# Kernel optimization log

Measured on AMD Instinct MI355X. Metric: run time of the kernel, lower is better.

The kernel has to match this reference:

```python
import jax, jax.numpy as jnp
import numpy as np
from jax import lax

M = 8192  # number of candidate detections
C = 80    # number of classes (COCO)
MIN_CONF = 0.25
MIN_IOU = 0.45
VALID_CLASS_IDS = jnp.array([2, 3, 5, 7], dtype=jnp.int32)  # COCO vehicles


def setup_inputs() -> dict:
    key = jax.random.key(0)
    k1, k2, k3, k4, k5, k6, k7 = jax.random.split(key, 7)
    # boxes stored as (y1, x1, y2, x2) in input-image pixel space, guaranteed y1<y2, x1<x2
    y1 = jax.random.uniform(k1, (1, M)) * 600.0
    x1 = jax.random.uniform(k2, (1, M)) * 600.0
    h = jax.random.uniform(k3, (1, M)) * 120.0 + 4.0
    w = jax.random.uniform(k4, (1, M)) * 120.0 + 4.0
    boxes_raw = jnp.stack([y1, x1, y1 + h, x1 + w], axis=-1).astype(jnp.float32)  # [1,M,4]
    scores = jax.random.uniform(k5, (1, C, M), dtype=jnp.float32)  # [1,C,M]
    cls = jax.random.randint(k6, (1, M), 0, C, dtype=jnp.int32)
    idx = jax.random.randint(k7, (1, M), 0, M, dtype=jnp.int32)
    indices = jnp.stack([jnp.zeros_like(cls), cls, idx], axis=-1)  # [1,M,3]: (batch, class_id, box_idx)
    return {"boxes_raw": boxes_raw, "scores": scores, "indices": indices, "out_h": 640, "out_w": 640}


def _pairwise_iou(b):
    # b: [M,4] (x1,y1,x2,y2)
    x1, y1, x2, y2 = b[:, 0], b[:, 1], b[:, 2], b[:, 3]
    area = jnp.maximum(x2 - x1, 0.0) * jnp.maximum(y2 - y1, 0.0)  # [M]
    ix1 = jnp.maximum(x1[:, None], x1[None, :])
    iy1 = jnp.maximum(y1[:, None], y1[None, :])
    ix2 = jnp.minimum(x2[:, None], x2[None, :])
    iy2 = jnp.minimum(y2[:, None], y2[None, :])
    inter = jnp.maximum(ix2 - ix1, 0.0) * jnp.maximum(iy2 - iy1, 0.0)  # [M,M]
    return inter / (area[:, None] + area[None, :] - inter + 1e-9)


def _postprocess(boxes_raw, scores, indices, out_h, out_w):
    idxs = indices[0, :, 2]       # predicted-positive box indices [M]
    class_ids = indices[0, :, 1]  # class ids [M]
    conf = scores[0, class_ids, idxs]  # irregular gather [M]
    b = boxes_raw[0, idxs]  # [M,4] (y1,x1,y2,x2)
    # swap to (x1,y1,x2,y2) as in the original column permutation
    boxes = jnp.stack([b[:, 1], b[:, 0], b[:, 3], b[:, 2]], axis=-1)
    bounds = jnp.array([out_w, out_h, out_w, out_h], dtype=boxes.dtype)
    boxes = jnp.clip(boxes, 0.0, bounds)  # clip_boxes to output image size
    # confidence filter + class filter (as masks; static shapes)
    valid = (conf > MIN_CONF) & jnp.isin(class_ids, VALID_CLASS_IDS)
    # class-agnostic greedy NMS over valid detections
    s = jnp.where(valid, conf, -1.0)
    order = jnp.argsort(-s)  # descending score
    sb = boxes[order]
    sv = valid[order]
    iou = _pairwise_iou(sb)  # [M,M]
    rng = jnp.arange(M)

    def body(i, keep):
        suppress = keep[i] & (iou[i] > MIN_IOU) & (rng > i)
        return keep & ~suppress

    keep_sorted = lax.fori_loop(0, M, body, sv)
    keep = jnp.zeros((M,), dtype=bool).at[order].set(keep_sorted)
    boxes_out = boxes * keep[:, None].astype(boxes.dtype)
    conf_out = conf * keep.astype(conf.dtype)
    return boxes_out, conf_out, class_ids.astype(jnp.int64), keep


def reference(boxes_raw, scores, indices, out_h, out_w):
    return _postprocess(boxes_raw, scores, indices, out_h, out_w)
```

## Files before the change

kernel.cpp:

```cpp
#include <hip/hip_runtime.h>
#include <stdint.h>

#define M_BOXES 8192
#define MIN_CONF_F 0.25f
#define MIN_IOU_F 0.45f
#define VCAP 640
#define NW 10
#define NBLKB 32
#define FLAG_MAGIC 0x5EEDF00D

typedef unsigned long long u64;
typedef unsigned int u32;

#define WS_FLAGS  0
#define WS_WCNT   512
#define WS_VKEYS  1024
#define WS_SUP    66560
#define WS_NEED   117760

__device__ inline float scalar_to_float(const int* p) {
    int v = p[0];
    if (v > 0 && v < (1 << 20)) return (float)v;
    return __int_as_float(v);
}

__device__ inline u64 rl64(u64 v, int b) {
    u32 lo = (u32)__builtin_amdgcn_readlane((int)(u32)v, b);
    u32 hi = (u32)__builtin_amdgcn_readlane((int)(u32)(v >> 32), b);
    return ((u64)hi << 32) | lo;
}

__device__ inline u64 rfl64(u64 v) {
    u32 lo = (u32)__builtin_amdgcn_readfirstlane((int)(u32)v);
    u32 hi = (u32)__builtin_amdgcn_readfirstlane((int)(u32)(v >> 32));
    return ((u64)hi << 32) | lo;
}

__device__ inline u64 wave_or64(u64 v) {
    #pragma unroll
    for (int o = 32; o > 0; o >>= 1) {
        int lo = __shfl_xor((int)(u32)v, o, 64);
        int hi = __shfl_xor((int)(u32)(v >> 32), o, 64);
        v |= ((u64)(u32)hi << 32) | (u32)lo;
    }
    return v;
}

__global__ __launch_bounds__(512) void kA_gather(
    const float* __restrict__ scores, const int* __restrict__ indices,
    float* __restrict__ out, u64* __restrict__ vkeys, int* __restrict__ wcnt)
{
    int tid = threadIdx.x;
    int i = blockIdx.x * 512 + tid;
    int cls = indices[3 * i + 1];
    int idx = indices[3 * i + 2];
    float conf = scores[cls * M_BOXES + idx];
    *reinterpret_cast<float4*>(out + 4 * i) = make_float4(0.f, 0.f, 0.f, 0.f);
    out[4 * M_BOXES + i] = 0.f;
    out[5 * M_BOXES + i] = (float)cls;
    out[6 * M_BOXES + i] = 0.f;
    bool valid = (conf > MIN_CONF_F) &&
                 (cls == 2 || cls == 3 || cls == 5 || cls == 7);
    u64 mask = __ballot(valid);
    int lane = tid & 63;
    int wid = i >> 6;
    if (valid) {
        int pos = (int)__popcll(mask & ((1ull << lane) - 1ull));
        u64 key = ((u64)(~__float_as_uint(conf)) << 32)
                | ((u64)(u32)i << 13) | (u64)(u32)idx;
        vkeys[(wid << 6) + pos] = key;
    }
    if (lane == 0) wcnt[wid] = (int)__popcll(mask);
}

__global__ __launch_bounds__(512) void kB_all(
    const float* __restrict__ boxes_raw, const int* __restrict__ p_out_h,
    const int* __restrict__ p_out_w, float* __restrict__ out,
    const u64* __restrict__ vkeys, const int* __restrict__ wcnt,
    u64* __restrict__ sup, int* __restrict__ flags)
{
    __shared__ int pre_s[129];
    __shared__ u64 tkey[VCAP];
    __shared__ u64 skey_s[VCAP];
    __shared__ float4 sbox_s[VCAP];
    __shared__ float sarea_s[VCAP];
    __shared__ u64 live_s[NW];

    int tid = threadIdx.x, b = blockIdx.x;
    int widx = tid >> 6, lane = tid & 63;

    if (tid < 64) {
        int cA = wcnt[tid], cB = wcnt[64 + tid];
        int sA = cA, sB = cB;
        #pragma unroll
        for (int o = 1; o < 64; o <<= 1) {
            int t = __shfl_up(sA, o, 64); if (tid >= o) sA += t;
            int u = __shfl_up(sB, o, 64); if (tid >= o) sB += u;
        }
        int totA = __shfl(sA, 63, 64);
        int totB = __shfl(sB, 63, 64);
        pre_s[tid] = sA - cA;
        pre_s[64 + tid] = totA + sB - cB;
        if (tid == 0) pre_s[128] = totA + totB;
    }
    __syncthreads();
    int V = pre_s[128];
    if (V > VCAP) V = VCAP;

    if (V > 0) {
        for (int s = tid; s < V; s += 512) {
            int lo = 0, hi = 128;
            #pragma unroll
            for (int st = 0; st < 7; ++st) {
                int mid = (lo + hi) >> 1;
                if (pre_s[mid] <= s) lo = mid; else hi = mid;
            }
            tkey[s] = vkeys[(lo << 6) + (s - pre_s[lo])];
        }
        __syncthreads();

        float W = scalar_to_float(p_out_w);
        float H = scalar_to_float(p_out_h);
        for (int s = tid; s < V; s += 512) {
            u64 k = tkey[s];
            int bidx = (int)(k & 0x1FFFull);
            float4 bb = *reinterpret_cast<const float4*>(boxes_raw + 4 * bidx);
            int r = 0;
            #pragma unroll 4
            for (int j = 0; j < V; ++j) r += (tkey[j] < k) ? 1 : 0;
            float4 c4;
            c4.x = fminf(fmaxf(bb.y, 0.f), W);
            c4.y = fminf(fmaxf(bb.x, 0.f), H);
            c4.z = fminf(fmaxf(bb.w, 0.f), W);
            c4.w = fminf(fmaxf(bb.z, 0.f), H);
            skey_s[r] = k;
            sbox_s[r] = c4;
            sarea_s[r] = fmaxf(c4.z - c4.x, 0.f) * fmaxf(c4.w - c4.y, 0.f);
        }
        __syncthreads();

        int nw = (V + 63) >> 6;
        int nbi = (V + 7) >> 3;
        int ntask = nbi * nw;
        int gw = (b << 3) + widx;
        for (int t = gw; t < ntask; t += NBLKB * 8) {
            int bi = t / nw;
            int w = t - bi * nw;
            int i0 = bi << 3;
            int j = (w << 6) + lane;
            bool jv = j < V;
            float4 bj = jv ? sbox_s[j] : make_float4(0.f, 0.f, 0.f, 0.f);
            float aj = jv ? sarea_s[j] : 0.f;
            int rend = V - i0; if (rend > 8) rend = 8;
            for (int r = 0; r < rend; ++r) {
                int i = i0 + r;
                float4 bi4 = sbox_s[i];
                float ai = sarea_s[i];
                bool p = false;
                if (jv && j > i) {
                    float ix1 = fmaxf(bi4.x, bj.x);
                    float iy1 = fmaxf(bi4.y, bj.y);
                    float ix2 = fminf(bi4.z, bj.z);
                    float iy2 = fminf(bi4.w, bj.w);
                    float inter = fmaxf(ix2 - ix1, 0.f) * fmaxf(iy2 - iy1, 0.f);
                    float iou = inter / (ai + aj - inter + 1e-9f);
                    p = iou > MIN_IOU_F;
                }
                u64 bits = __ballot(p);
                if (lane == 0) sup[i * NW + w] = bits;
            }
        }
    }

    __syncthreads();
    if (tid == 0) {
        __threadfence();
        __hip_atomic_store(&flags[b], FLAG_MAGIC, __ATOMIC_RELEASE,
                           __HIP_MEMORY_SCOPE_AGENT);
    }
    if (b != 0) return;
    if (tid < NBLKB) {
        while (__hip_atomic_load(&flags[tid], __ATOMIC_ACQUIRE,
                                 __HIP_MEMORY_SCOPE_AGENT) != FLAG_MAGIC)
            __builtin_amdgcn_s_sleep(1);
    }
    __syncthreads();
    __threadfence();

    if (V > 0) {
        int nw = (V + 63) >> 6;
        if (tid < 64) {
            u64 live[NW], supp[NW];
            #pragma unroll
            for (int w = 0; w < NW; ++w) {
                int c = V - (w << 6);
                live[w] = (c >= 64) ? ~0ull : (c > 0 ? ((1ull << c) - 1ull) : 0ull);
                supp[w] = 0ull;
            }
            u64 rowA[NW], rowB[NW];
            {
                bool rv = lane < V;
                #pragma unroll
                for (int w = 0; w < NW; ++w)
                    rowA[w] = (rv && w < nw) ? sup[lane * NW + w] : 0ull;
            }
            auto step = [&](u64 (&rc)[NW], u64 (&rn)[NW], int ci) {
                int rI = ((ci + 1) << 6) + lane;
                bool rv = (ci + 1) < nw && rI < V;
                #pragma unroll
                for (int w = 0; w < NW; ++w)
                    rn[w] = (rv && w >= ci + 1 && w < nw) ? sup[rI * NW + w] : 0ull;
                u64 rw = 0, cur = 0;
                #pragma unroll
                for (int w = 0; w < NW; ++w)
                    if (w == ci) { rw = rc[w]; cur = live[w] & ~supp[w]; }
                cur = rfl64(cur);
                #pragma unroll
                for (int bb = 0; bb < 64; ++bb) {
                    u64 rb = rl64(rw, bb);
                    u64 nxt = cur & ~rb;
                    cur = ((cur >> bb) & 1ull) ? nxt : cur;
                }
                #pragma unroll
                for (int w = 0; w < NW; ++w) if (w == ci) live[w] = cur;
                #pragma unroll
                for (int w2 = 0; w2 < NW; ++w2)
                    if (w2 > ci && w2 < nw) {
                        u64 mine = ((cur >> lane) & 1ull) ? rc[w2] : 0ull;
                        supp[w2] |= rfl64(wave_or64(mine));
                    }
            };
            int ci = 0;
            while (ci < nw) {
                step(rowA, rowB, ci); ++ci;
                if (ci < nw) { step(rowB, rowA, ci); ++ci; }
            }
            #pragma unroll
            for (int w = 0; w < NW; ++w) live_s[w] = live[w];
        }
        __syncthreads();
        for (int s = tid; s < V; s += 512) {
            if ((live_s[s >> 6] >> (s & 63)) & 1ull) {
                u64 k = skey_s[s];
                u32 orig = (u32)((k >> 13) & 0x1FFFull);
                float conf = __uint_as_float(~(u32)(k >> 32));
                float4 bb = sbox_s[s];
                *reinterpret_cast<float4*>(out + 4 * orig) = bb;
                out[4 * M_BOXES + orig] = conf;
                out[6 * M_BOXES + orig] = 1.0f;
            }
        }
    }

    if (tid < NBLKB)
        __hip_atomic_store(&flags[tid], 0, __ATOMIC_RELEASE,
                           __HIP_MEMORY_SCOPE_AGENT);
}

__global__ __launch_bounds__(256) void fb_gather(
    const float* __restrict__ boxes_raw, const float* __restrict__ scores,
    const int* __restrict__ indices, const int* __restrict__ p_out_h,
    const int* __restrict__ p_out_w, float* __restrict__ out,
    u64* __restrict__ vkeys, float4* __restrict__ vboxes,
    int* __restrict__ vcount)
{
    int i = blockIdx.x * blockDim.x + threadIdx.x;
    if (i >= M_BOXES) return;
    int cls = indices[3 * i + 1];
    int idx = indices[3 * i + 2];
    float conf = scores[cls * M_BOXES + idx];
    *reinterpret_cast<float4*>(out + 4 * i) = make_float4(0.f, 0.f, 0.f, 0.f);
    out[4 * M_BOXES + i] = 0.f;
    out[5 * M_BOXES + i] = (float)cls;
    out[6 * M_BOXES + i] = 0.f;
    bool valid = (conf > MIN_CONF_F) &&
                 (cls == 2 || cls == 3 || cls == 5 || cls == 7);
    if (valid) {
        float4 bb = *reinterpret_cast<const float4*>(boxes_raw + 4 * idx);
        float W = scalar_to_float(p_out_w);
        float H = scalar_to_float(p_out_h);
        float4 c;
        c.x = fminf(fmaxf(bb.y, 0.f), W);
        c.y = fminf(fmaxf(bb.x, 0.f), H);
        c.z = fminf(fmaxf(bb.w, 0.f), W);
        c.w = fminf(fmaxf(bb.z, 0.f), H);
        int p = atomicAdd(vcount, 1);
        if (p < VCAP) {
            vkeys[p] = ((u64)(~__float_as_uint(conf)) << 32) | (u32)i;
            vboxes[p] = c;
        }
    }
}

__global__ __launch_bounds__(1024) void fb_nms(
    float* __restrict__ out, const u64* __restrict__ vkeys,
    const float4* __restrict__ vboxes, const int* __restrict__ vcount)
{
    __shared__ u64 tkey[VCAP];
    __shared__ u64 skey[VCAP];
    __shared__ float4 sbox[VCAP];
    __shared__ unsigned char keepb[VCAP];
    int tid = threadIdx.x;
    int V = *vcount;
    if (V > VCAP) V = VCAP;
    if (V <= 0) return;
    for (int s = tid; s < V; s += 1024) tkey[s] = vkeys[s];
    __syncthreads();
    for (int s = tid; s < V; s += 1024) {
        u64 k = tkey[s];
        int r = 0;
        for (int j = 0; j < V; ++j) r += (tkey[j] < k);
        skey[r] = k;
        sbox[r] = vboxes[s];
    }
    __syncthreads();
    for (int s = tid; s < V; s += 1024) keepb[s] = 1;
    __syncthreads();
    for (int i = 0; i < V; ++i) {
        if (keepb[i]) {
            float4 bi = sbox[i];
            float ai = fmaxf(bi.z - bi.x, 0.f) * fmaxf(bi.w - bi.y, 0.f);
            for (int s = i + 1 + tid; s < V; s += 1024) {
                if (keepb[s]) {
                    float4 bj = sbox[s];
                    float aj = fmaxf(bj.z - bj.x, 0.f) * fmaxf(bj.w - bj.y, 0.f);
                    float ix1 = fmaxf(bi.x, bj.x);
                    float iy1 = fmaxf(bi.y, bj.y);
                    float ix2 = fminf(bi.z, bj.z);
                    float iy2 = fminf(bi.w, bj.w);
                    float inter = fmaxf(ix2 - ix1, 0.f) * fmaxf(iy2 - iy1, 0.f);
                    float iou = inter / (ai + aj - inter + 1e-9f);
                    if (iou > MIN_IOU_F) keepb[s] = 0;
                }
            }
        }
        __syncthreads();
    }
    for (int s = tid; s < V; s += 1024) {
        if (keepb[s]) {
            u64 k = skey[s];
            u32 orig = (u32)(k & 0xFFFFFFFFull);
            float conf = __uint_as_float(~(u32)(k >> 32));
            float4 bb = sbox[s];
            *reinterpret_cast<float4*>(out + 4 * orig) = bb;
            out[4 * M_BOXES + orig] = conf;
            out[6 * M_BOXES + orig] = 1.0f;
        }
    }
}

extern "C" void kernel_launch(void* const* d_in, const int* in_sizes, int n_in,
                              void* d_out, int out_size, void* d_ws, size_t ws_size,
                              hipStream_t stream) {
    const float* boxes_raw = (const float*)d_in[0];
    const float* scores    = (const float*)d_in[1];
    const int*   indices   = (const int*)d_in[2];
    const int*   p_out_h   = (const int*)d_in[3];
    const int*   p_out_w   = (const int*)d_in[4];
    float* out = (float*)d_out;
    char* ws = (char*)d_ws;

    if (ws_size >= WS_NEED) {
        int* flags = (int*)(ws + WS_FLAGS);
        int* wcnt  = (int*)(ws + WS_WCNT);
        u64* vkeys = (u64*)(ws + WS_VKEYS);
        u64* sup   = (u64*)(ws + WS_SUP);

        kA_gather<<<M_BOXES / 512, 512, 0, stream>>>(
            scores, indices, out, vkeys, wcnt);
        kB_all<<<NBLKB, 512, 0, stream>>>(
            boxes_raw, p_out_h, p_out_w, out, vkeys, wcnt, sup, flags);
    } else {
        int*    vcount = (int*)ws;
        u64*    vkeys  = (u64*)(ws + 16);
        float4* vboxes = (float4*)(ws + 16 + VCAP * sizeof(u64));
        hipMemsetAsync(d_ws, 0, 16, stream);
        fb_gather<<<M_BOXES / 256, 256, 0, stream>>>(
            boxes_raw, scores, indices, p_out_h, p_out_w, out,
            vkeys, vboxes, vcount);
        fb_nms<<<1, 1024, 0, stream>>>(out, vkeys, vboxes, vcount);
    }
}
```

Baseline: 35.41 us.

## Fuse gather kernel into NMS kernel with a grid-wide flag barrier

Merges the score gather/compaction kernel into the main NMS kernel. Each of the 32 blocks gathers 256 candidates, then all blocks spin on a second set of release/acquire flags before the prefix scan. This removes one kernel launch and the inter-kernel gap, at the cost of a software grid barrier that only works if all 32 blocks are co-resident. Half of each block's threads sit idle during the gather phase.

New measurement: 38.18 us. 1.08x slower.

```diff
diff --git a/kernel.cpp b/kernel.cpp
--- a/kernel.cpp
+++ b/kernel.cpp
@@ -6,13 +6,14 @@
 #define MIN_IOU_F 0.45f
 #define VCAP 640
 #define NW 10
-#define NBLKB 32
+#define NBLK 32
 #define FLAG_MAGIC 0x5EEDF00D
 
 typedef unsigned long long u64;
 typedef unsigned int u32;
 
-#define WS_FLAGS  0
+#define WS_FA     0
+#define WS_FC     128
 #define WS_WCNT   512
 #define WS_VKEYS  1024
 #define WS_SUP    66560
@@ -46,38 +47,12 @@
     return v;
 }
 
-__global__ __launch_bounds__(512) void kA_gather(
-    const float* __restrict__ scores, const int* __restrict__ indices,
-    float* __restrict__ out, u64* __restrict__ vkeys, int* __restrict__ wcnt)
-{
-    int tid = threadIdx.x;
-    int i = blockIdx.x * 512 + tid;
-    int cls = indices[3 * i + 1];
-    int idx = indices[3 * i + 2];
-    float conf = scores[cls * M_BOXES + idx];
-    *reinterpret_cast<float4*>(out + 4 * i) = make_float4(0.f, 0.f, 0.f, 0.f);
-    out[4 * M_BOXES + i] = 0.f;
-    out[5 * M_BOXES + i] = (float)cls;
-    out[6 * M_BOXES + i] = 0.f;
-    bool valid = (conf > MIN_CONF_F) &&
-                 (cls == 2 || cls == 3 || cls == 5 || cls == 7);
-    u64 mask = __ballot(valid);
-    int lane = tid & 63;
-    int wid = i >> 6;
-    if (valid) {
-        int pos = (int)__popcll(mask & ((1ull << lane) - 1ull));
-        u64 key = ((u64)(~__float_as_uint(conf)) << 32)
-                | ((u64)(u32)i << 13) | (u64)(u32)idx;
-        vkeys[(wid << 6) + pos] = key;
-    }
-    if (lane == 0) wcnt[wid] = (int)__popcll(mask);
-}
-
-__global__ __launch_bounds__(512) void kB_all(
-    const float* __restrict__ boxes_raw, const int* __restrict__ p_out_h,
+__global__ __launch_bounds__(512) void kONE2(
+    const float* __restrict__ boxes_raw, const float* __restrict__ scores,
+    const int* __restrict__ indices, const int* __restrict__ p_out_h,
     const int* __restrict__ p_out_w, float* __restrict__ out,
-    const u64* __restrict__ vkeys, const int* __restrict__ wcnt,
-    u64* __restrict__ sup, int* __restrict__ flags)
+    u64* __restrict__ vkeys, int* __restrict__ wcnt,
+    u64* __restrict__ sup, int* __restrict__ fA, int* __restrict__ fC)
 {
     __shared__ int pre_s[129];
     __shared__ u64 tkey[VCAP];
@@ -88,6 +63,42 @@
 
     int tid = threadIdx.x, b = blockIdx.x;
     int widx = tid >> 6, lane = tid & 63;
+
+    if (tid < 256) {
+        int i = (b << 8) + tid;
+        int cls = indices[3 * i + 1];
+        int idx = indices[3 * i + 2];
+        float conf = scores[cls * M_BOXES + idx];
+        *reinterpret_cast<float4*>(out + 4 * i) = make_float4(0.f, 0.f, 0.f, 0.f);
+        out[4 * M_BOXES + i] = 0.f;
+        out[5 * M_BOXES + i] = (float)cls;
+        out[6 * M_BOXES + i] = 0.f;
+        bool valid = (conf > MIN_CONF_F) &&
+                     (cls == 2 || cls == 3 || cls == 5 || cls == 7);
+        u64 mask = __ballot(valid);
+        int wid = i >> 6;
+        if (valid) {
+            int pos = (int)__popcll(mask & ((1ull << lane) - 1ull));
+            u64 key = ((u64)(~__float_as_uint(conf)) << 32)
+                    | ((u64)(u32)i << 13) | (u64)(u32)idx;
+            vkeys[(wid << 6) + pos] = key;
+        }
+        if (lane == 0) wcnt[wid] = (int)__popcll(mask);
+    }
+
+    __syncthreads();
+    if (tid == 0) {
+        __threadfence();
+        __hip_atomic_store(&fA[b], FLAG_MAGIC, __ATOMIC_RELEASE,
+                           __HIP_MEMORY_SCOPE_AGENT);
+    }
+    if (tid < NBLK) {
+        while (__hip_atomic_load(&fA[tid], __ATOMIC_ACQUIRE,
+                                 __HIP_MEMORY_SCOPE_AGENT) != FLAG_MAGIC)
+            __builtin_amdgcn_s_sleep(1);
+    }
+    __syncthreads();
+    __threadfence();
 
     if (tid < 64) {
         int cA = wcnt[tid], cB = wcnt[64 + tid];
@@ -143,7 +154,7 @@
         int nbi = (V + 7) >> 3;
         int ntask = nbi * nw;
         int gw = (b << 3) + widx;
-        for (int t = gw; t < ntask; t += NBLKB * 8) {
+        for (int t = gw; t < ntask; t += NBLK * 8) {
             int bi = t / nw;
             int w = t - bi * nw;
             int i0 = bi << 3;
@@ -175,12 +186,12 @@
     __syncthreads();
     if (tid == 0) {
         __threadfence();
-        __hip_atomic_store(&flags[b], FLAG_MAGIC, __ATOMIC_RELEASE,
+        __hip_atomic_store(&fC[b], FLAG_MAGIC, __ATOMIC_RELEASE,
                            __HIP_MEMORY_SCOPE_AGENT);
     }
     if (b != 0) return;
-    if (tid < NBLKB) {
-        while (__hip_atomic_load(&flags[tid], __ATOMIC_ACQUIRE,
+    if (tid < NBLK) {
+        while (__hip_atomic_load(&fC[tid], __ATOMIC_ACQUIRE,
                                  __HIP_MEMORY_SCOPE_AGENT) != FLAG_MAGIC)
             __builtin_amdgcn_s_sleep(1);
     }
@@ -252,9 +263,10 @@
         }
     }
 
-    if (tid < NBLKB)
-        __hip_atomic_store(&flags[tid], 0, __ATOMIC_RELEASE,
-                           __HIP_MEMORY_SCOPE_AGENT);
+    if (tid < NBLK) {
+        __hip_atomic_store(&fA[tid], 0, __ATOMIC_RELEASE, __HIP_MEMORY_SCOPE_AGENT);
+        __hip_atomic_store(&fC[tid], 0, __ATOMIC_RELEASE, __HIP_MEMORY_SCOPE_AGENT);
+    }
 }
 
 __global__ __launch_bounds__(256) void fb_gather(
@@ -361,15 +373,15 @@
     char* ws = (char*)d_ws;
 
     if (ws_size >= WS_NEED) {
-        int* flags = (int*)(ws + WS_FLAGS);
+        int* fA    = (int*)(ws + WS_FA);
+        int* fC    = (int*)(ws + WS_FC);
         int* wcnt  = (int*)(ws + WS_WCNT);
         u64* vkeys = (u64*)(ws + WS_VKEYS);
         u64* sup   = (u64*)(ws + WS_SUP);
 
-        kA_gather<<<M_BOXES / 512, 512, 0, stream>>>(
-            scores, indices, out, vkeys, wcnt);
-        kB_all<<<NBLKB, 512, 0, stream>>>(
-            boxes_raw, p_out_h, p_out_w, out, vkeys, wcnt, sup, flags);
+        kONE2<<<NBLK, 512, 0, stream>>>(
+            boxes_raw, scores, indices, p_out_h, p_out_w, out,
+            vkeys, wcnt, sup, fA, fC);
     } else {
         int*    vcount = (int*)ws;
         u64*    vkeys  = (u64*)(ws + 16);
```
